# Performance work log

Measured on AMD Instinct MI355X. Metric: run time of the kernel, lower is better.

## Reference

```python
import jax, jax.numpy as jnp
import numpy as np

DN = ('NCHW', 'OIHW', 'NCHW')
B, C, H, W = 4, 64, 256, 256
MIP = 8          # max(8, C // 32)
RED = C // 16    # CBAM reduced channels
PS = 8           # FSAS patch size


def conv2d(x, w, padding=0, groups=1):
    return jax.lax.conv_general_dilated(
        x, w, (1, 1), [(padding, padding), (padding, padding)],
        dimension_numbers=DN, feature_group_count=groups)


def bn_eval(x, g, b, eps=1e-5):
    # BatchNorm with init running stats (mean=0, var=1), eval mode
    return x / jnp.sqrt(1.0 + eps) * g[None, :, None, None] + b[None, :, None, None]


def h_swish(x):
    return x * jnp.clip(x + 3.0, 0.0, 6.0) / 6.0


def setup_inputs() -> dict:
    key = jax.random.key(0)
    ks = jax.random.split(key, 12)
    s = 0.05
    d = {
        'x': jax.random.normal(ks[0], (B, C, H, W), jnp.float32),
        # CoordAttention
        'ca_conv1_w': jax.random.normal(ks[1], (MIP, C, 1, 1), jnp.float32) * s,
        'ca_conv1_b': jnp.zeros((MIP,), jnp.float32),
        'ca_bn_g': jnp.ones((MIP,), jnp.float32),
        'ca_bn_b': jnp.zeros((MIP,), jnp.float32),
        'ca_convh_w': jax.random.normal(ks[2], (C, MIP, 1, 1), jnp.float32) * s,
        'ca_convh_b': jnp.zeros((C,), jnp.float32),
        'ca_convw_w': jax.random.normal(ks[3], (C, MIP, 1, 1), jnp.float32) * s,
        'ca_convw_b': jnp.zeros((C,), jnp.float32),
        # FSAS (bias=False)
        'fsas_hidden_w': jax.random.normal(ks[4], (6 * C, C, 1, 1), jnp.float32) * s,
        'fsas_dw_w': jax.random.normal(ks[5], (6 * C, 1, 3, 3), jnp.float32) * s,
        'fsas_proj_w': jax.random.normal(ks[6], (C, 2 * C, 1, 1), jnp.float32) * s,
        'ln_w': jnp.ones((2 * C,), jnp.float32),
        'ln_b': jnp.zeros((2 * C,), jnp.float32),
        # Fusion
        'fus_conv1_w': jax.random.normal(ks[7], (2 * C, 2 * C, 3, 3), jnp.float32) * s,
        'fus_bn1_g': jnp.ones((2 * C,), jnp.float32),
        'fus_bn1_b': jnp.zeros((2 * C,), jnp.float32),
        'fus_conv2_w': jax.random.normal(ks[8], (C, 2 * C, 1, 1), jnp.float32) * s,
        'fus_bn2_g': jnp.ones((C,), jnp.float32),
        'fus_bn2_b': jnp.zeros((C,), jnp.float32),
        # CBAM
        'cbam_mlp1_w': jax.random.normal(ks[9], (RED, C, 1, 1), jnp.float32) * s,
        'cbam_mlp2_w': jax.random.normal(ks[10], (C, RED, 1, 1), jnp.float32) * s,
        'cbam_sa_w': jax.random.normal(ks[11], (1, 2, 7, 7), jnp.float32) * s,
        'residual_scale': jnp.float32(0.1),
    }
    return d


def _forward(x, ca_conv1_w, ca_conv1_b, ca_bn_g, ca_bn_b, ca_convh_w, ca_convh_b,
             ca_convw_w, ca_convw_b, fsas_hidden_w, fsas_dw_w, fsas_proj_w, ln_w, ln_b,
             fus_conv1_w, fus_bn1_g, fus_bn1_b, fus_conv2_w, fus_bn2_g, fus_bn2_b,
             cbam_mlp1_w, cbam_mlp2_w, cbam_sa_w, residual_scale):
    b, c, h, w = x.shape
    c2 = 2 * c

    # ---- CoordAttention branch ----
    xh = jnp.mean(x, axis=3, keepdims=True)                       # [B,C,H,1]
    xw = jnp.mean(x, axis=2, keepdims=True).transpose(0, 1, 3, 2)  # [B,C,W,1]
    y = jnp.concatenate([xh, xw], axis=2)                          # [B,C,H+W,1]
    y = conv2d(y, ca_conv1_w) + ca_conv1_b[None, :, None, None]
    y = h_swish(bn_eval(y, ca_bn_g, ca_bn_b))
    yh, yw = y[:, :, :h], y[:, :, h:]
    yw = yw.transpose(0, 1, 3, 2)
    a_h = jax.nn.sigmoid(conv2d(yh, ca_convh_w) + ca_convh_b[None, :, None, None])
    a_w = jax.nn.sigmoid(conv2d(yw, ca_convw_w) + ca_convw_b[None, :, None, None])
    ca_out = x * a_h * a_w

    # ---- FSAS branch ----
    hid = conv2d(x, fsas_hidden_w)                                 # [B,6C,H,W]
    hid = conv2d(hid, fsas_dw_w, padding=1, groups=6 * c)          # depthwise 3x3
    q, k, v = jnp.split(hid, 3, axis=1)                            # each [B,2C,H,W]

    def patch(t):  # [B,2C,H,W] -> [B,2C,H/8,W/8,8,8]
        return t.reshape(b, c2, h // PS, PS, w // PS, PS).transpose(0, 1, 2, 4, 3, 5)

    qf = jnp.fft.rfft2(patch(q))
    kf = jnp.fft.rfft2(patch(k))
    o = jnp.fft.irfft2(qf * kf, s=(PS, PS))
    o = o.transpose(0, 1, 2, 4, 3, 5).reshape(b, c2, h, w)

    # WithBias LayerNorm over channel dim (per pixel)
    mu = jnp.mean(o, axis=1, keepdims=True)
    var = jnp.var(o, axis=1, keepdims=True)
    on = (o - mu) / jnp.sqrt(var + 1e-5) * ln_w[None, :, None, None] + ln_b[None, :, None, None]
    fsas_out = conv2d(v * on, fsas_proj_w)                         # [B,C,H,W]

    # ---- Fusion ----
    f = conv2d(jnp.concatenate([ca_out, fsas_out], axis=1), fus_conv1_w, padding=1)
    f = jax.nn.gelu(bn_eval(f, fus_bn1_g, fus_bn1_b), approximate=False)
    f = bn_eval(conv2d(f, fus_conv2_w), fus_bn2_g, fus_bn2_b)

    z = x + residual_scale * f

    # ---- CBAM ----
    avg = jnp.mean(z, axis=(2, 3), keepdims=True)
    mx = jnp.max(z, axis=(2, 3), keepdims=True)

    def mlp(t):
        return conv2d(jax.nn.relu(conv2d(t, cbam_mlp1_w)), cbam_mlp2_w)

    z = z * jax.nn.sigmoid(mlp(avg) + mlp(mx))
    sa = jnp.concatenate([jnp.mean(z, axis=1, keepdims=True),
                          jnp.max(z, axis=1, keepdims=True)], axis=1)
    z = z * jax.nn.sigmoid(conv2d(sa, cbam_sa_w, padding=3))
    return jax.nn.gelu(z, approximate=False)


def reference(x, ca_conv1_w, ca_conv1_b, ca_bn_g, ca_bn_b, ca_convh_w, ca_convh_b,
              ca_convw_w, ca_convw_b, fsas_hidden_w, fsas_dw_w, fsas_proj_w, ln_w, ln_b,
              fus_conv1_w, fus_bn1_g, fus_bn1_b, fus_conv2_w, fus_bn2_g, fus_bn2_b,
              cbam_mlp1_w, cbam_mlp2_w, cbam_sa_w, residual_scale):
    return _forward(x, ca_conv1_w, ca_conv1_b, ca_bn_g, ca_bn_b, ca_convh_w, ca_convh_b,
                    ca_convw_w, ca_convw_b, fsas_hidden_w, fsas_dw_w, fsas_proj_w, ln_w, ln_b,
                    fus_conv1_w, fus_bn1_g, fus_bn1_b, fus_conv2_w, fus_bn2_g, fus_bn2_b,
                    cbam_mlp1_w, cbam_mlp2_w, cbam_sa_w, residual_scale)
```

## Files before the change

kernel.cpp:

```cpp
#include <hip/hip_runtime.h>
#include <math.h>

#define B_ 4
#define C_ 64
#define C2_ 128
#define C6_ 384
#define H_ 256
#define Wd_ 256
#define HW_ 65536
#define MIP_ 8
#define BNINV 0.9999950000374994f

typedef short bf16x8 __attribute__((ext_vector_type(8)));
typedef float f32x4 __attribute__((ext_vector_type(4)));
typedef unsigned short u16x8 __attribute__((ext_vector_type(8)));
typedef unsigned short u16x4 __attribute__((ext_vector_type(4)));
typedef unsigned int   u32x4 __attribute__((ext_vector_type(4)));

__device__ __forceinline__ float sigm(float x){ return 1.f/(1.f+expf(-x)); }
__device__ __forceinline__ float gelu_f(float x){ return 0.5f*x*(1.f+erff(x*0.7071067811865476f)); }
__device__ __forceinline__ unsigned short bfrnd(float f){
  unsigned u = __float_as_uint(f);
  unsigned r = u + 0x7FFFu + ((u>>16)&1u);
  return (unsigned short)(r>>16);
}
__device__ __forceinline__ float bf2f(unsigned short s){
  return __uint_as_float(((unsigned)s)<<16);
}

__global__ void __launch_bounds__(256) k_xstat(const float* __restrict__ x,
                                               float* __restrict__ xh, float* __restrict__ xw){
  int plane = blockIdx.x;
  int tid = threadIdx.x;
  const float* p = x + (size_t)plane*HW_;
  float cs = 0.f;
  for(int h=0;h<256;h++) cs += p[h*256+tid];
  xw[plane*256+tid] = cs*(1.f/256.f);
  float rs = 0.f;
  const f32x4* pr4 = (const f32x4*)(p + (size_t)tid*256);
  #pragma unroll 8
  for(int w=0;w<64;w++){ f32x4 v = pr4[w]; rs += v[0]+v[1]+v[2]+v[3]; }
  xh[plane*256+tid] = rs*(1.f/256.f);
}

__global__ void k_ca_t(const float* __restrict__ xh, const float* __restrict__ xw,
                       const float* __restrict__ w1, const float* __restrict__ b1,
                       const float* __restrict__ bng, const float* __restrict__ bnb,
                       float* __restrict__ t){
  int idx = blockIdx.x*256 + threadIdx.x;
  int p = idx & 511; int m = (idx>>9)&7; int b = idx>>12;
  float acc = b1[m];
  #pragma unroll 8
  for(int c=0;c<C_;c++){
    float yv = (p<256) ? xh[(b*C_+c)*256 + p] : xw[(b*C_+c)*256 + (p-256)];
    acc += w1[m*C_+c]*yv;
  }
  float v = acc*BNINV*bng[m] + bnb[m];
  t[idx] = v * fminf(fmaxf(v+3.f,0.f),6.f)*(1.f/6.f);
}

__global__ void k_ca_a(const float* __restrict__ t,
                       const float* __restrict__ wh, const float* __restrict__ bh,
                       const float* __restrict__ ww, const float* __restrict__ bw,
                       float* __restrict__ ah, float* __restrict__ aw){
  int idx = blockIdx.x*256 + threadIdx.x;
  int p = idx & 511; int co = (idx>>9)&63; int b = idx>>15;
  bool isH = (p<256);
  const float* wm = isH ? wh : ww;
  float acc = isH ? bh[co] : bw[co];
  #pragma unroll
  for(int m=0;m<MIP_;m++) acc += wm[co*MIP_+m]*t[(b*MIP_+m)*512+p];
  float s = sigm(acc);
  if(isH) ah[(b*C_+co)*256+p] = s; else aw[(b*C_+co)*256+(p-256)] = s;
}

__global__ void __launch_bounds__(256) k_xprep(const float* __restrict__ x, unsigned short* __restrict__ xb){
  __shared__ float sm[64][65];
  int tid = threadIdx.x;
  int img = blockIdx.x >> 10;
  int p0 = (blockIdx.x & 1023)*64;
  int lane = tid & 63, wq = tid >> 6;
  #pragma unroll
  for(int cc=0; cc<16; ++cc){
    int c = cc*4 + wq;
    sm[c][lane] = x[(size_t)(img*C_+c)*HW_ + p0 + lane];
  }
  __syncthreads();
  int pl = tid >> 2;
  int c0 = (tid & 3) * 16;
  u16x8 lo, hi;
  #pragma unroll
  for(int i=0;i<8;i++)  lo[i] = bfrnd(sm[c0+i][pl]);
  #pragma unroll
  for(int i=0;i<8;i++)  hi[i] = bfrnd(sm[c0+8+i][pl]);
  unsigned short* dst = xb + ((size_t)img*HW_ + p0 + pl)*64 + c0;
  *(u16x8*)(dst)     = lo;
  *(u16x8*)(dst + 8) = hi;
}

__global__ void k_wprep(const float* __restrict__ w, unsigned short* __restrict__ wbt){
  int t = blockIdx.x*256 + threadIdx.x;
  const float* src = w + (size_t)t*9;
  int oc = t >> 7, ic = t & 127;
  #pragma unroll
  for(int tap=0; tap<9; ++tap)
    wbt[(size_t)(tap*128+oc)*128 + ic] = bfrnd(src[tap]);
}

__global__ void k_wprep2(const float* __restrict__ pw, const float* __restrict__ w2,
                         const float* __restrict__ hw, unsigned short* __restrict__ pwb,
                         unsigned short* __restrict__ w2b, unsigned short* __restrict__ wb1){
  int t = blockIdx.x*256 + threadIdx.x;
  if(t < 8192){ pwb[t] = bfrnd(pw[t]); w2b[t] = bfrnd(w2[t]); }
  wb1[t] = bfrnd(hw[t]);
}

__global__ void __launch_bounds__(256) k_hid0_mfma(const unsigned short* __restrict__ xb,
                                                   const unsigned short* __restrict__ wb1,
                                                   unsigned short* __restrict__ hid0b){
  int tid = threadIdx.x;
  int lane = tid & 63, wid = tid >> 6;
  int l15 = lane & 15, lk = lane >> 4;
  int p0 = blockIdx.x*128 + wid*32;
  int oc0 = blockIdx.y*96;
  f32x4 acc[6][2];
  #pragma unroll
  for(int m=0;m<6;m++)
    #pragma unroll
    for(int n=0;n<2;n++) acc[m][n] = (f32x4)0.f;
  #pragma unroll
  for(int kk=0; kk<2; ++kk){
    bf16x8 bfr[2];
    #pragma unroll
    for(int n=0;n<2;n++)
      bfr[n] = *(const bf16x8*)(xb + (size_t)(p0 + n*16 + l15)*64 + kk*32 + lk*8);
    #pragma unroll
    for(int m=0;m<6;m++){
      bf16x8 af = *(const bf16x8*)(wb1 + (size_t)(oc0 + m*16 + l15)*64 + kk*32 + lk*8);
      #pragma unroll
      for(int n=0;n<2;n++)
        acc[m][n] = __builtin_amdgcn_mfma_f32_16x16x32_bf16(af, bfr[n], acc[m][n], 0,0,0);
    }
  }
  #pragma unroll
  for(int n=0;n<2;n++){
    int p = p0 + n*16 + l15;
    #pragma unroll
    for(int m=0;m<6;m++){
      u16x4 v;
      #pragma unroll
      for(int r=0;r<4;r++) v[r] = bfrnd(acc[m][n][r]);
      *(u16x4*)(hid0b + (size_t)p*384 + oc0 + m*16 + lk*4) = v;
    }
  }
}

__global__ void __launch_bounds__(256) k_dw_bf(const unsigned short* __restrict__ hid0b,
                                               const float* __restrict__ wd,
                                               unsigned short* __restrict__ hidb){
  int tid = threadIdx.x;
  int cg = tid & 15;
  int tg = tid >> 4;
  int p0 = blockIdx.x*64;
  int h  = p0 >> 8;
  int w0 = (p0 & 255) + tg*4;
  int chb = blockIdx.y*128 + cg*8;

  float wreg[72];
  {
    const f32x4* wsrc = (const f32x4*)(wd + (size_t)chb*9);
    #pragma unroll
    for(int i=0;i<18;i++){
      f32x4 v = wsrc[i];
      wreg[4*i+0]=v[0]; wreg[4*i+1]=v[1]; wreg[4*i+2]=v[2]; wreg[4*i+3]=v[3];
    }
  }
  float acc[4][8];
  #pragma unroll
  for(int px=0;px<4;px++)
    #pragma unroll
    for(int e=0;e<8;e++) acc[px][e] = 0.f;

  #pragma unroll
  for(int ky=0; ky<3; ++ky){
    int hh = h + ky - 1;
    if((unsigned)hh >= 256u) continue;
    float row[6][8];
    #pragma unroll
    for(int c6=0; c6<6; ++c6){
      int ww = w0 + c6 - 1;
      u16x8 v8 = {0,0,0,0,0,0,0,0};
      if((unsigned)ww < 256u)
        v8 = *(const u16x8*)(hid0b + (size_t)(hh*256+ww)*384 + chb);
      #pragma unroll
      for(int e=0;e<8;e++) row[c6][e] = bf2f(v8[e]);
    }
    #pragma unroll
    for(int kx=0; kx<3; ++kx){
      #pragma unroll
      for(int px=0; px<4; ++px){
        #pragma unroll
        for(int e=0;e<8;e++)
          acc[px][e] += row[px+kx][e] * wreg[e*9 + ky*3 + kx];
      }
    }
  }
  #pragma unroll
  for(int px=0; px<4; ++px){
    u16x8 o8;
    #pragma unroll
    for(int e=0;e<8;e++) o8[e] = bfrnd(acc[px][e]);
    *(u16x8*)(hidb + (size_t)(p0 + tg*4 + px)*384 + chb) = o8;
  }
}

__global__ void __launch_bounds__(256) k_circ_bf(const unsigned short* __restrict__ hidb,
                                                 unsigned short* __restrict__ ob){
  __shared__ __align__(16) unsigned short lq[2][64][128];
  __shared__ __align__(16) unsigned short lkk[2][64][128];
  int tid = threadIdx.x;
  #pragma unroll
  for(int it=0; it<8; ++it){
    int s = it*256 + tid;
    int which = s >> 10, rem = s & 1023;
    int pix = rem >> 4, cg = rem & 15;
    int gp = blockIdx.x*2 + which;
    int ph = gp >> 5, pw = gp & 31;
    size_t pg = (size_t)((ph*8 + (pix>>3))*256 + pw*8 + (pix&7));
    *(u16x8*)&lq[which][pix][cg*8]  = *(const u16x8*)(hidb + pg*384 + cg*8);
    *(u16x8*)&lkk[which][pix][cg*8] = *(const u16x8*)(hidb + pg*384 + 128 + cg*8);
  }
  __syncthreads();
  int which = tid >> 7, c = tid & 127;
  float kr[64];
  #pragma unroll
  for(int pix=0;pix<64;pix++) kr[pix] = bf2f(lkk[which][pix][c]);
  float outv[64];
  #pragma unroll
  for(int t2=0;t2<64;t2++) outv[t2] = 0.f;
  #pragma unroll
  for(int u=0;u<8;u++){
    #pragma unroll
    for(int v=0;v<8;v++){
      float qv = bf2f(lq[which][u*8+v][c]);
      #pragma unroll
      for(int i=0;i<8;i++){
        #pragma unroll
        for(int j=0;j<8;j++)
          outv[i*8+j] += qv * kr[((i-u)&7)*8 + ((j-v)&7)];
      }
    }
  }
  __syncthreads();
  #pragma unroll
  for(int t2=0;t2<64;t2++) lq[which][t2][c] = bfrnd(outv[t2]);
  __syncthreads();
  #pragma unroll
  for(int it=0; it<8; ++it){
    int s = it*256 + tid;
    int which2 = s >> 10, rem = s & 1023;
    int pix = rem >> 4, cg = rem & 15;
    int gp = blockIdx.x*2 + which2;
    int ph = gp >> 5, pw = gp & 31;
    size_t pg = (size_t)((ph*8 + (pix>>3))*256 + pw*8 + (pix&7));
    *(u16x8*)(ob + pg*128 + cg*8) = *(u16x8*)&lq[which2][pix][cg*8];
  }
}

__global__ void __launch_bounds__(256) k_proj_mfma(const unsigned short* __restrict__ ob,
                      const unsigned short* __restrict__ hidb,
                      const float* __restrict__ lnw, const float* __restrict__ lnb,
                      const unsigned short* __restrict__ pwb, unsigned short* __restrict__ catb){
  __shared__ unsigned int lds32[256*64];
  int tid = threadIdx.x;
  int lane = tid & 63, wid = tid >> 6;
  int p0 = blockIdx.x*256;
  {
    int p = p0 + tid;
    u16x8 o8[16];
    #pragma unroll
    for(int g=0; g<16; ++g) o8[g] = *(const u16x8*)(ob + (size_t)p*128 + g*8);
    float s=0.f, s2=0.f;
    #pragma unroll
    for(int g=0; g<16; ++g)
      #pragma unroll
      for(int e=0; e<8; ++e){ float v = bf2f(o8[g][e]); s += v; s2 += v*v; }
    float m = s*(1.f/C2_);
    float var = s2*(1.f/C2_) - m*m;
    float rs = rsqrtf(var + 1e-5f);
    #pragma unroll
    for(int cg=0; cg<16; ++cg){
      u16x8 v8 = *(const u16x8*)(hidb + (size_t)p*384 + 256 + cg*8);
      unsigned uu[4];
      #pragma unroll
      for(int ee=0; ee<4; ++ee){
        int c = cg*8 + ee*2;
        float on0 = (bf2f(o8[cg][2*ee])   - m)*rs*lnw[c]   + lnb[c];
        float on1 = (bf2f(o8[cg][2*ee+1]) - m)*rs*lnw[c+1] + lnb[c+1];
        float vn0 = bf2f(v8[2*ee])*on0;
        float vn1 = bf2f(v8[2*ee+1])*on1;
        uu[ee] = (unsigned)bfrnd(vn0) | ((unsigned)bfrnd(vn1)<<16);
      }
      int blk = cg ^ (tid & 15);
      u32x4 w4 = {uu[0],uu[1],uu[2],uu[3]};
      *(u32x4*)&lds32[tid*64 + blk*4] = w4;
    }
  }
  __syncthreads();
  int l15 = lane & 15, lk = lane >> 4;
  f32x4 acc[4][4];
  #pragma unroll
  for(int m=0;m<4;m++)
    #pragma unroll
    for(int n=0;n<4;n++) acc[m][n] = (f32x4)0.f;
  int plb = wid*64;
  #pragma unroll
  for(int kk=0; kk<4; ++kk){
    bf16x8 bfr[4];
    #pragma unroll
    for(int n=0;n<4;n++){
      int pl = plb + n*16 + l15;
      int blk = (kk*4 + lk) ^ l15;
      bfr[n] = *(bf16x8*)&lds32[pl*64 + blk*4];
    }
    #pragma unroll
    for(int m=0;m<4;m++){
      bf16x8 af = *(const bf16x8*)(pwb + (size_t)(m*16+l15)*128 + kk*32 + lk*8);
      #pragma unroll
      for(int n=0;n<4;n++)
        acc[m][n] = __builtin_amdgcn_mfma_f32_16x16x32_bf16(af, bfr[n], acc[m][n], 0,0,0);
    }
  }
  #pragma unroll
  for(int n=0;n<4;n++){
    int p = p0 + plb + n*16 + l15;
    #pragma unroll
    for(int m=0;m<4;m++){
      u16x4 v;
      #pragma unroll
      for(int r=0;r<4;r++) v[r] = bfrnd(acc[m][n][r]);
      *(u16x4*)(catb + (size_t)p*128 + 64 + m*16 + lk*4) = v;
    }
  }
}

__global__ void __launch_bounds__(256) k_caout_bf(const float* __restrict__ x, const float* __restrict__ ah,
                        const float* __restrict__ aw, unsigned short* __restrict__ catb, int b){
  __shared__ float sm[64][65];
  int tid = threadIdx.x;
  int p0 = blockIdx.x*64;
  int h = p0 >> 8;
  int wbase = p0 & 255;
  int lane = tid & 63, wq = tid >> 6;
  #pragma unroll
  for(int cc=0; cc<16; ++cc){
    int c = cc*4 + wq;
    float v = x[(size_t)(b*C_+c)*HW_ + p0 + lane];
    v *= ah[(b*C_+c)*256 + h] * aw[(b*C_+c)*256 + wbase + lane];
    sm[c][lane] = v;
  }
  __syncthreads();
  int pl = tid >> 2;
  int c0 = (tid & 3) * 16;
  u16x8 lo, hi;
  #pragma unroll
  for(int i=0;i<8;i++)  lo[i] = bfrnd(sm[c0+i][pl]);
  #pragma unroll
  for(int i=0;i<8;i++)  hi[i] = bfrnd(sm[c0+8+i][pl]);
  unsigned short* dst = catb + (size_t)(p0+pl)*128 + c0;
  *(u16x8*)(dst)     = lo;
  *(u16x8*)(dst + 8) = hi;
}

__global__ void __launch_bounds__(256,3) k_fus1_mfma(const unsigned short* __restrict__ catb,
                                                     const unsigned short* __restrict__ wbt,
                                                     unsigned short* __restrict__ f1b){
  __shared__ __align__(16) unsigned short sA[3][130][32];
  int tid = threadIdx.x;
  int lane = tid & 63, wid = tid >> 6;
  int wm = wid & 1, wn = wid >> 1;
  int bid = blockIdx.x;
  int xcd = bid & 7, idx = bid >> 3;
  int h   = xcd*32 + (idx >> 2);
  int w0  = ((idx >> 1) & 1) * 128;
  int ocb = (idx & 1) * 64 + wn*32;
  int l15 = lane & 15, lk = lane >> 4;

  int srow[7], spxl[7], sicq[7];
  bool sok[7], sld[7];
  #pragma unroll
  for(int it=0; it<7; ++it){
    int s = it*256 + tid;
    sok[it] = (s < 1560);
    int row = s/520;
    int rem = s - row*520;
    int pxl = rem >> 2;
    int icq = rem & 3;
    srow[it]=row; spxl[it]=pxl; sicq[it]=icq;
    int r = h + row - 1;
    int c = w0 + pxl - 1;
    sld[it] = sok[it] && (unsigned)r < 256u && (unsigned)c < 256u;
  }

  u16x8 st[7];
  #pragma unroll
  for(int it=0; it<7; ++it){
    u16x8 v = {0,0,0,0,0,0,0,0};
    if(sld[it]){
      int r = h + srow[it] - 1, c = w0 + spxl[it] - 1;
      v = *(const u16x8*)(catb + (size_t)(r*256 + c)*128 + sicq[it]*8);
    }
    st[it] = v;
  }

  f32x4 acc[4][2];
  #pragma unroll
  for(int i=0;i<4;i++)
    #pragma unroll
    for(int j=0;j<2;j++) acc[i][j] = (f32x4)0.f;

  const unsigned short* wbase = wbt + (size_t)(ocb + l15)*128 + lk*8;

  for(int icc=0; icc<4; ++icc){
    int ic0 = icc*32;
    __syncthreads();
    #pragma unroll
    for(int it=0; it<7; ++it){
      if(sok[it]){
        int blk = sicq[it] ^ ((spxl[it]>>1)&3);
        *(u16x8*)&sA[srow[it]][spxl[it]][blk*8] = st[it];
      }
    }
    __syncthreads();
    if(icc < 3){
      int ic0n = (icc+1)*32;
      #pragma unroll
      for(int it=0; it<7; ++it){
        u16x8 v = {0,0,0,0,0,0,0,0};
        if(sld[it]){
          int r = h + srow[it] - 1, c = w0 + spxl[it] - 1;
          v = *(const u16x8*)(catb + (size_t)(r*256 + c)*128 + ic0n + sicq[it]*8);
        }
        st[it] = v;
      }
    }
    #pragma unroll
    for(int ky=0; ky<3; ++ky){
      bf16x8 wf[3][2];
      #pragma unroll
      for(int kx=0; kx<3; ++kx){
        const unsigned short* wt = wbase + (size_t)(ky*3+kx)*16384 + ic0;
        wf[kx][0] = *(const bf16x8*)(wt);
        wf[kx][1] = *(const bf16x8*)(wt + 2048);
      }
      #pragma unroll
      for(int kx=0; kx<3; ++kx){
        #pragma unroll
        for(int i=0;i<4;++i){
          int rr = wm*64 + i*16 + l15 + kx;
          int blk = lk ^ ((rr>>1)&3);
          bf16x8 a = *(const bf16x8*)&sA[ky][rr][blk*8];
          acc[i][0] = __builtin_amdgcn_mfma_f32_16x16x32_bf16(wf[kx][0], a, acc[i][0], 0,0,0);
          acc[i][1] = __builtin_amdgcn_mfma_f32_16x16x32_bf16(wf[kx][1], a, acc[i][1], 0,0,0);
        }
      }
    }
  }
  #pragma unroll
  for(int i=0;i<4;i++){
    int sp = h*256 + w0 + wm*64 + i*16 + l15;
    #pragma unroll
    for(int j=0;j<2;j++){
      u16x4 v;
      #pragma unroll
      for(int r2=0;r2<4;r2++) v[r2] = bfrnd(acc[i][j][r2]);
      *(u16x4*)(f1b + (size_t)sp*128 + ocb + j*16 + lk*4) = v;
    }
  }
}

__global__ void __launch_bounds__(256) k_fus2_mfma(const unsigned short* __restrict__ f1b,
                      const float* __restrict__ x, const unsigned short* __restrict__ w2b,
                      const float* __restrict__ bn1g, const float* __restrict__ bn1b,
                      const float* __restrict__ bn2g, const float* __restrict__ bn2b,
                      const float* __restrict__ rscale, unsigned short* __restrict__ zb,
                      float* __restrict__ psum2, float* __restrict__ pmax2, int b){
  __shared__ unsigned int lds32[128*64];
  __shared__ float smp[4][4][16], smm[4][4][16];
  int tid = threadIdx.x;
  int lane = tid & 63, wid = tid >> 6;
  int p0 = blockIdx.x*128;
  int ic0 = (tid & 15) * 8;
  #pragma unroll
  for(int pass=0; pass<8; ++pass){
    int pl = pass*16 + (tid>>4);
    bf16x8 vv = *(const bf16x8*)(f1b + (size_t)(p0+pl)*128 + ic0);
    unsigned uu[4];
    #pragma unroll
    for(int ee=0; ee<4; ++ee){
      float f0 = bf2f((unsigned short)vv[2*ee])  *BNINV*bn1g[ic0+2*ee]   + bn1b[ic0+2*ee];
      float f1 = bf2f((unsigned short)vv[2*ee+1])*BNINV*bn1g[ic0+2*ee+1] + bn1b[ic0+2*ee+1];
      uu[ee] = (unsigned)bfrnd(gelu_f(f0)) | ((unsigned)bfrnd(gelu_f(f1))<<16);
    }
    int blk = (ic0>>3) ^ (pl&15);
    u32x4 w4 = {uu[0],uu[1],uu[2],uu[3]};
    *(u32x4*)&lds32[pl*64 + blk*4] = w4;
  }
  __syncthreads();
  int l15 = lane & 15, lk = lane >> 4;
  f32x4 acc[4][2];
  #pragma unroll
  for(int m=0;m<4;m++)
    #pragma unroll
    for(int n=0;n<2;n++) acc[m][n] = (f32x4)0.f;
  int pl0 = wid*32 + l15;
  #pragma unroll
  for(int kk=0; kk<4; ++kk){
    bf16x8 bfr[2];
    #pragma unroll
    for(int n=0;n<2;n++){
      int pl = pl0 + n*16;
      int blk = (kk*4 + lk) ^ l15;
      bfr[n] = *(bf16x8*)&lds32[pl*64 + blk*4];
    }
    #pragma unroll
    for(int m=0;m<4;m++){
      bf16x8 af = *(const bf16x8*)(w2b + (size_t)(m*16+l15)*128 + kk*32 + lk*8);
      #pragma unroll
      for(int n=0;n<2;n++)
        acc[m][n] = __builtin_amdgcn_mfma_f32_16x16x32_bf16(af, bfr[n], acc[m][n], 0,0,0);
    }
  }
  float rs = rscale[0];
  float ps[4][4], pm[4][4];
  #pragma unroll
  for(int m=0;m<4;m++)
    #pragma unroll
    for(int r=0;r<4;r++){ ps[m][r]=0.f; pm[m][r]=-INFINITY; }
  #pragma unroll
  for(int n=0;n<2;n++){
    int p = p0 + pl0 + n*16;
    #pragma unroll
    for(int m=0;m<4;m++){
      #pragma unroll
      for(int r=0;r<4;r++){
        int oc = m*16 + lk*4 + r;
        float f = acc[m][n][r]*BNINV*bn2g[oc] + bn2b[oc];
        float zv = x[(size_t)(b*C_+oc)*HW_ + p] + rs*f;
        zb[(size_t)oc*HW_ + p] = bfrnd(zv);
        ps[m][r] += zv; pm[m][r] = fmaxf(pm[m][r], zv);
      }
    }
  }
  #pragma unroll
  for(int off=1; off<16; off<<=1){
    #pragma unroll
    for(int m=0;m<4;m++)
      #pragma unroll
      for(int r=0;r<4;r++){
        ps[m][r] += __shfl_xor(ps[m][r], off, 64);
        pm[m][r] = fmaxf(pm[m][r], __shfl_xor(pm[m][r], off, 64));
      }
  }
  if(l15 == 0){
    #pragma unroll
    for(int m=0;m<4;m++)
      #pragma unroll
      for(int r=0;r<4;r++){
        smp[wid][lk][m*4+r] = ps[m][r];
        smm[wid][lk][m*4+r] = pm[m][r];
      }
  }
  __syncthreads();
  if(tid < 64){
    int m = tid>>4, lkg = (tid>>2)&3, r = tid&3;
    float s = 0.f, mx = -INFINITY;
    #pragma unroll
    for(int w=0;w<4;w++){
      s += smp[w][lkg][m*4+r];
      mx = fmaxf(mx, smm[w][lkg][m*4+r]);
    }
    psum2[blockIdx.x*64 + tid] = s;
    pmax2[blockIdx.x*64 + tid] = mx;
  }
}

__global__ void k_cbamred2(const float* __restrict__ psum2, const float* __restrict__ pmax2,
                           float* __restrict__ avgb4, float* __restrict__ maxb4){
  int c = blockIdx.x & 63; int b = blockIdx.x >> 6;
  const float* ps = psum2 + (size_t)b*32768;
  const float* pmx = pmax2 + (size_t)b*32768;
  int tid = threadIdx.x;
  float s = ps[(size_t)tid*64 + c] + ps[(size_t)(tid+256)*64 + c];
  float m = fmaxf(pmx[(size_t)tid*64 + c], pmx[(size_t)(tid+256)*64 + c]);
  __shared__ float ss[256], sm[256];
  ss[tid]=s; sm[tid]=m; __syncthreads();
  for(int off=128; off>0; off>>=1){
    if(tid<off){ ss[tid]+=ss[tid+off]; sm[tid]=fmaxf(sm[tid],sm[tid+off]); }
    __syncthreads();
  }
  if(tid==0){ avgb4[b*64+c]=ss[0]*(1.f/HW_); maxb4[b*64+c]=sm[0]; }
}

__global__ void k_cbammlp(const float* __restrict__ avgb4, const float* __restrict__ maxb4,
                          const float* __restrict__ w1, const float* __restrict__ w2,
                          float* __restrict__ catt4){
  __shared__ float h1s[4][8];
  int tid = threadIdx.x;
  int b = tid >> 6, cl = tid & 63;
  if(cl < 8){
    const float* src = (cl<4)? avgb4 + b*64 : maxb4 + b*64;
    int r = cl & 3;
    float s = 0.f;
    for(int c=0;c<C_;c++) s += w1[r*C_+c]*src[c];
    h1s[b][cl] = fmaxf(s,0.f);
  }
  __syncthreads();
  float a = 0.f;
  #pragma unroll
  for(int r=0;r<4;r++) a += w2[cl*4+r]*(h1s[b][r]+h1s[b][r+4]);
  catt4[b*64+cl] = sigm(a);
}

__global__ void k_chatt(const unsigned short* __restrict__ z4, const float* __restrict__ catt4,
                        float* __restrict__ samean4, float* __restrict__ samax4){
  int gp = blockIdx.x*256 + threadIdx.x;
  int b = gp >> 16; int p = gp & 65535;
  const unsigned short* zb = z4 + (size_t)b*C_*HW_;
  const float* ct = catt4 + b*64;
  float s = 0.f, m = -INFINITY;
  #pragma unroll 8
  for(int c=0;c<C_;c++){
    float v = bf2f(zb[(size_t)c*HW_+p])*ct[c];
    s += v; m = fmaxf(m,v);
  }
  samean4[gp] = s*(1.f/C_);
  samax4[gp] = m;
}

__global__ void k_saconv(const float* __restrict__ samean4, const float* __restrict__ samax4,
                         const float* __restrict__ saw, float* __restrict__ att4){
  int gp = blockIdx.x*256 + threadIdx.x;
  int b = gp >> 16; int p = gp & 65535;
  int base = b << 16;
  int h = p>>8, w = p&255;
  float acc = 0.f;
  #pragma unroll
  for(int ky=0;ky<7;ky++){
    int hh = h+ky-3; if((unsigned)hh>=256u) continue;
    #pragma unroll
    for(int kx=0;kx<7;kx++){
      int ww2 = w+kx-3; if((unsigned)ww2>=256u) continue;
      int q = base + hh*256+ww2;
      acc += samean4[q]*saw[ky*7+kx] + samax4[q]*saw[49+ky*7+kx];
    }
  }
  att4[gp] = sigm(acc);
}

__global__ void k_final(const unsigned short* __restrict__ z4, const float* __restrict__ catt4,
                        const float* __restrict__ att4, float* __restrict__ out){
  int gp = blockIdx.x*256 + threadIdx.x;
  int b = gp >> 16; int p = gp & 65535;
  int c = blockIdx.y;
  float v = bf2f(z4[((size_t)(b*C_+c))*HW_ + p]) * catt4[b*64+c] * att4[gp];
  out[((size_t)(b*C_+c))*HW_ + p] = gelu_f(v);
}

extern "C" void kernel_launch(void* const* d_in, const int* in_sizes, int n_in,
                              void* d_out, int out_size, void* d_ws, size_t ws_size,
                              hipStream_t stream){
  const float* x            = (const float*)d_in[0];
  const float* ca_conv1_w   = (const float*)d_in[1];
  const float* ca_conv1_b   = (const float*)d_in[2];
  const float* ca_bn_g      = (const float*)d_in[3];
  const float* ca_bn_b      = (const float*)d_in[4];
  const float* ca_convh_w   = (const float*)d_in[5];
  const float* ca_convh_b   = (const float*)d_in[6];
  const float* ca_convw_w   = (const float*)d_in[7];
  const float* ca_convw_b   = (const float*)d_in[8];
  const float* fsas_hidden_w= (const float*)d_in[9];
  const float* fsas_dw_w    = (const float*)d_in[10];
  const float* fsas_proj_w  = (const float*)d_in[11];
  const float* ln_w         = (const float*)d_in[12];
  const float* ln_b         = (const float*)d_in[13];
  const float* fus_conv1_w  = (const float*)d_in[14];
  const float* fus_bn1_g    = (const float*)d_in[15];
  const float* fus_bn1_b    = (const float*)d_in[16];
  const float* fus_conv2_w  = (const float*)d_in[17];
  const float* fus_bn2_g    = (const float*)d_in[18];
  const float* fus_bn2_b    = (const float*)d_in[19];
  const float* cbam_mlp1_w  = (const float*)d_in[20];
  const float* cbam_mlp2_w  = (const float*)d_in[21];
  const float* cbam_sa_w    = (const float*)d_in[22];
  const float* rscale       = (const float*)d_in[23];
  float* out = (float*)d_out;
  float* ws  = (float*)d_ws;

  float* xh      = ws + 0;
  float* xw      = ws + 65536;
  float* t       = ws + 131072;
  float* ah      = ws + 147456;
  float* aw      = ws + 212992;
  float* catt4   = ws + 278528;
  float* avgb4   = ws + 278784;
  float* maxb4   = ws + 279040;
  float* psum2   = ws + 279296;
  float* pmax2   = ws + 410368;
  float* samean4 = ws + 541440;
  float* samax4  = ws + 803584;
  float* att4    = ws + 1065728;
  float* big     = ws + 1327872;
  unsigned short* catb  = (unsigned short*)(big);
  unsigned short* f1b   = (unsigned short*)(big + 4194304);
  unsigned short* z4    = (unsigned short*)(big + 8388608);
  unsigned short* xb    = (unsigned short*)(big + 16777216);
  unsigned short* hid0b = (unsigned short*)(big + 25165824);
  unsigned short* hidb  = (unsigned short*)(big + 37748736);
  unsigned short* obuf  = (unsigned short*)(big + 50331648);
  unsigned short* wbt   = (unsigned short*)(big + 54525952);
  unsigned short* wb1   = (unsigned short*)(big + 54599680);
  unsigned short* pwb   = (unsigned short*)(big + 54611968);
  unsigned short* w2b   = (unsigned short*)(big + 54616064);

  k_xstat<<<256,256,0,stream>>>(x, xh, xw);
  k_ca_t<<<64,256,0,stream>>>(xh, xw, ca_conv1_w, ca_conv1_b, ca_bn_g, ca_bn_b, t);
  k_ca_a<<<512,256,0,stream>>>(t, ca_convh_w, ca_convh_b, ca_convw_w, ca_convw_b, ah, aw);
  k_xprep<<<4096,256,0,stream>>>(x, xb);
  k_wprep<<<64,256,0,stream>>>(fus_conv1_w, wbt);
  k_wprep2<<<96,256,0,stream>>>(fsas_proj_w, fus_conv2_w, fsas_hidden_w, pwb, w2b, wb1);

  for(int b=0;b<4;b++){
    k_hid0_mfma<<<dim3(512,4),256,0,stream>>>(xb + (size_t)b*HW_*64, wb1, hid0b);
    k_dw_bf<<<dim3(1024,3),256,0,stream>>>(hid0b, fsas_dw_w, hidb);
    k_circ_bf<<<512,256,0,stream>>>(hidb, obuf);
    k_proj_mfma<<<256,256,0,stream>>>(obuf, hidb, ln_w, ln_b, pwb, catb);
    k_caout_bf<<<1024,256,0,stream>>>(x, ah, aw, catb, b);
    k_fus1_mfma<<<1024,256,0,stream>>>(catb, wbt, f1b);
    k_fus2_mfma<<<512,256,0,stream>>>(f1b, x, w2b, fus_bn1_g, fus_bn1_b, fus_bn2_g, fus_bn2_b,
                                      rscale, z4 + (size_t)b*C_*HW_,
                                      psum2 + (size_t)b*32768, pmax2 + (size_t)b*32768, b);
  }

  k_cbamred2<<<256,256,0,stream>>>(psum2, pmax2, avgb4, maxb4);
  k_cbammlp<<<1,256,0,stream>>>(avgb4, maxb4, cbam_mlp1_w, cbam_mlp2_w, catt4);
  k_chatt<<<1024,256,0,stream>>>(z4, catt4, samean4, samax4);
  k_saconv<<<1024,256,0,stream>>>(samean4, samax4, cbam_sa_w, att4);
  k_final<<<dim3(1024,64),256,0,stream>>>(z4, catt4, att4, out);
}
```

Measured before the change: 766.6 us.

## Fuse hidden 1x1 conv into depthwise 3x3 conv via shared-memory halo tile

Merges the MFMA 1x1 hidden projection and the depthwise 3x3 conv into one kernel. Each block computes the 1x1 output for a 3-row by 66-column halo tile of 128 channels into LDS, then runs the depthwise conv from LDS. This removes the global write and re-read of the 384-channel intermediate buffer and one launch per batch. In exchange it recomputes the 1x1 conv on halo pixels (about 3x rows plus edge columns), uses about 54KB of LDS, which may limit occupancy, and leaves some lanes idle in the tile loop.

Result: slower. 838.6 us (+9.4%).

```diff
diff --git a/kernel.cpp b/kernel.cpp
--- a/kernel.cpp
+++ b/kernel.cpp
@@ -115,57 +115,51 @@
   wb1[t] = bfrnd(hw[t]);
 }
 
-__global__ void __launch_bounds__(256) k_hid0_mfma(const unsigned short* __restrict__ xb,
-                                                   const unsigned short* __restrict__ wb1,
-                                                   unsigned short* __restrict__ hid0b){
+__global__ void __launch_bounds__(256) k_hiddw(const unsigned short* __restrict__ xb,
+                                               const unsigned short* __restrict__ wb1,
+                                               const float* __restrict__ wd,
+                                               unsigned short* __restrict__ hidb){
+  __shared__ __align__(16) unsigned short sH[3][66][136];
   int tid = threadIdx.x;
   int lane = tid & 63, wid = tid >> 6;
   int l15 = lane & 15, lk = lane >> 4;
-  int p0 = blockIdx.x*128 + wid*32;
-  int oc0 = blockIdx.y*96;
-  f32x4 acc[6][2];
-  #pragma unroll
-  for(int m=0;m<6;m++)
-    #pragma unroll
-    for(int n=0;n<2;n++) acc[m][n] = (f32x4)0.f;
-  #pragma unroll
-  for(int kk=0; kk<2; ++kk){
-    bf16x8 bfr[2];
-    #pragma unroll
-    for(int n=0;n<2;n++)
-      bfr[n] = *(const bf16x8*)(xb + (size_t)(p0 + n*16 + l15)*64 + kk*32 + lk*8);
-    #pragma unroll
-    for(int m=0;m<6;m++){
-      bf16x8 af = *(const bf16x8*)(wb1 + (size_t)(oc0 + m*16 + l15)*64 + kk*32 + lk*8);
-      #pragma unroll
-      for(int n=0;n<2;n++)
-        acc[m][n] = __builtin_amdgcn_mfma_f32_16x16x32_bf16(af, bfr[n], acc[m][n], 0,0,0);
-    }
-  }
-  #pragma unroll
-  for(int n=0;n<2;n++){
-    int p = p0 + n*16 + l15;
-    #pragma unroll
-    for(int m=0;m<6;m++){
-      u16x4 v;
-      #pragma unroll
-      for(int r=0;r<4;r++) v[r] = bfrnd(acc[m][n][r]);
-      *(u16x4*)(hid0b + (size_t)p*384 + oc0 + m*16 + lk*4) = v;
-    }
-  }
-}
-
-__global__ void __launch_bounds__(256) k_dw_bf(const unsigned short* __restrict__ hid0b,
-                                               const float* __restrict__ wd,
-                                               unsigned short* __restrict__ hidb){
-  int tid = threadIdx.x;
+  int p0 = blockIdx.x*64;
+  int h  = p0 >> 8;
+  int w0 = p0 & 255;
+  int ocb = blockIdx.y*128;
+
+  const unsigned short* wA0 = wb1 + (size_t)(ocb + (wid*2+0)*16 + l15)*64 + lk*8;
+  const unsigned short* wA1 = wb1 + (size_t)(ocb + (wid*2+1)*16 + l15)*64 + lk*8;
+  #pragma unroll
+  for(int pos=0; pos<15; ++pos){
+    int row = pos/5, nt = pos - (pos/5)*5;
+    int rg = h + row - 1;
+    int px_local = nt*16 + l15;
+    int colg = w0 - 1 + px_local;
+    bool ok = ((unsigned)rg < 256u) && ((unsigned)colg < 256u);
+    f32x4 a0 = (f32x4)0.f, a1 = (f32x4)0.f;
+    #pragma unroll
+    for(int kk=0; kk<2; ++kk){
+      bf16x8 bfr = {0,0,0,0,0,0,0,0};
+      if(ok) bfr = *(const bf16x8*)(xb + (size_t)(rg*256 + colg)*64 + kk*32 + lk*8);
+      bf16x8 af0 = *(const bf16x8*)(wA0 + kk*32);
+      bf16x8 af1 = *(const bf16x8*)(wA1 + kk*32);
+      a0 = __builtin_amdgcn_mfma_f32_16x16x32_bf16(af0, bfr, a0, 0,0,0);
+      a1 = __builtin_amdgcn_mfma_f32_16x16x32_bf16(af1, bfr, a1, 0,0,0);
+    }
+    if(px_local < 66){
+      u16x4 v0, v1;
+      #pragma unroll
+      for(int r=0;r<4;r++){ v0[r]=bfrnd(a0[r]); v1[r]=bfrnd(a1[r]); }
+      *(u16x4*)&sH[row][px_local][(wid*2+0)*16 + lk*4] = v0;
+      *(u16x4*)&sH[row][px_local][(wid*2+1)*16 + lk*4] = v1;
+    }
+  }
+  __syncthreads();
+
   int cg = tid & 15;
   int tg = tid >> 4;
-  int p0 = blockIdx.x*64;
-  int h  = p0 >> 8;
-  int w0 = (p0 & 255) + tg*4;
-  int chb = blockIdx.y*128 + cg*8;
-
+  int chb = ocb + cg*8;
   float wreg[72];
   {
     const f32x4* wsrc = (const f32x4*)(wd + (size_t)chb*9);
@@ -183,17 +177,12 @@
 
   #pragma unroll
   for(int ky=0; ky<3; ++ky){
-    int hh = h + ky - 1;
-    if((unsigned)hh >= 256u) continue;
-    float row[6][8];
+    float row6[6][8];
     #pragma unroll
     for(int c6=0; c6<6; ++c6){
-      int ww = w0 + c6 - 1;
-      u16x8 v8 = {0,0,0,0,0,0,0,0};
-      if((unsigned)ww < 256u)
-        v8 = *(const u16x8*)(hid0b + (size_t)(hh*256+ww)*384 + chb);
-      #pragma unroll
-      for(int e=0;e<8;e++) row[c6][e] = bf2f(v8[e]);
+      u16x8 v8 = *(const u16x8*)&sH[ky][tg*4 + c6][cg*8];
+      #pragma unroll
+      for(int e=0;e<8;e++) row6[c6][e] = bf2f(v8[e]);
     }
     #pragma unroll
     for(int kx=0; kx<3; ++kx){
@@ -201,7 +190,7 @@
       for(int px=0; px<4; ++px){
         #pragma unroll
         for(int e=0;e<8;e++)
-          acc[px][e] += row[px+kx][e] * wreg[e*9 + ky*3 + kx];
+          acc[px][e] += row6[px+kx][e] * wreg[e*9 + ky*3 + kx];
       }
     }
   }
@@ -715,13 +704,12 @@
   unsigned short* f1b   = (unsigned short*)(big + 4194304);
   unsigned short* z4    = (unsigned short*)(big + 8388608);
   unsigned short* xb    = (unsigned short*)(big + 16777216);
-  unsigned short* hid0b = (unsigned short*)(big + 25165824);
-  unsigned short* hidb  = (unsigned short*)(big + 37748736);
-  unsigned short* obuf  = (unsigned short*)(big + 50331648);
-  unsigned short* wbt   = (unsigned short*)(big + 54525952);
-  unsigned short* wb1   = (unsigned short*)(big + 54599680);
-  unsigned short* pwb   = (unsigned short*)(big + 54611968);
-  unsigned short* w2b   = (unsigned short*)(big + 54616064);
+  unsigned short* hidb  = (unsigned short*)(big + 25165824);
+  unsigned short* obuf  = (unsigned short*)(big + 37748736);
+  unsigned short* wbt   = (unsigned short*)(big + 41943040);
+  unsigned short* wb1   = (unsigned short*)(big + 42016768);
+  unsigned short* pwb   = (unsigned short*)(big + 42029056);
+  unsigned short* w2b   = (unsigned short*)(big + 42033152);
 
   k_xstat<<<256,256,0,stream>>>(x, xh, xw);
   k_ca_t<<<64,256,0,stream>>>(xh, xw, ca_conv1_w, ca_conv1_b, ca_bn_g, ca_bn_b, t);
@@ -731,8 +719,7 @@
   k_wprep2<<<96,256,0,stream>>>(fsas_proj_w, fus_conv2_w, fsas_hidden_w, pwb, w2b, wb1);
 
   for(int b=0;b<4;b++){
-    k_hid0_mfma<<<dim3(512,4),256,0,stream>>>(xb + (size_t)b*HW_*64, wb1, hid0b);
-    k_dw_bf<<<dim3(1024,3),256,0,stream>>>(hid0b, fsas_dw_w, hidb);
+    k_hiddw<<<dim3(1024,3),256,0,stream>>>(xb + (size_t)b*HW_*64, wb1, fsas_dw_w, hidb);
     k_circ_bf<<<512,256,0,stream>>>(hidb, obuf);
     k_proj_mfma<<<256,256,0,stream>>>(obuf, hidb, ln_w, ln_b, pwb, catb);
     k_caout_bf<<<1024,256,0,stream>>>(x, ah, aw, catb, b);
```
